# Performance work log

Measured on AMD Instinct MI355X. Metric: run time of the kernel, lower is better.

The kernel has to match this reference:

```python
import jax, jax.numpy as jnp
import numpy as np
from jax import lax

IN_CH, OUT_CH, KS, GROUPS = 64, 64, 3, 8
FPG = IN_CH // GROUPS  # features per group = 8
PAD = KS // 2


def setup_inputs() -> dict:
    key = jax.random.key(0)
    k1, k2, k3 = jax.random.split(key, 3)
    x = jax.random.normal(k1, (8, IN_CH, 256, 256), dtype=jnp.float32)
    representation = jax.random.normal(k2, (8, 32), dtype=jnp.float32)
    # Linear(32, OUT_CH*KS*KS, bias=False) weight, torch layout (out_features, in_features)
    W = jax.random.normal(k3, (OUT_CH * KS * KS, 32), dtype=jnp.float32) * (1.0 / np.sqrt(32))
    return {"x": x, "representation": representation, "W": W}


def reference(x, representation, W):
    b = x.shape[0]
    # ReflectionPad2d
    xp = jnp.pad(x, ((0, 0), (0, 0), (PAD, PAD), (PAD, PAD)), mode="reflect")
    # compress_key: Linear (no bias) + LeakyReLU(0.1)
    k = jax.nn.leaky_relu(representation @ W.T, 0.1)  # [b, OUT_CH*KS*KS]
    kernel = k.reshape(b, OUT_CH, 1, KS, KS)
    # repeat_interleave on a size-1 dim == broadcast/tile
    kernel = jnp.broadcast_to(kernel, (b, OUT_CH, FPG, KS, KS))
    # per-sample grouped conv (equivalent to torch's batch-as-groups trick)
    def conv_one(xi, ki):
        # xi: [C,H,W], ki: [OUT_CH, FPG, KS, KS]
        out = lax.conv_general_dilated(
            xi[None], ki, window_strides=(1, 1), padding="VALID",
            dimension_numbers=("NCHW", "OIHW", "NCHW"),
            feature_group_count=GROUPS)
        return out[0]
    return jax.vmap(conv_one)(xp, kernel)  # [b, OUT_CH, H, W]
```

## Files before the change

kernel.cpp:

```cpp
#include <hip/hip_runtime.h>


#define LDSW 68

__device__ __forceinline__ int reflect1(int i, int n) {
  if (i < 0) i = -i;
  if (i >= n) i = 2 * n - 2 - i;
  return i;
}

__global__ __launch_bounds__(256) void gsum_kernel(
    const float* __restrict__ x,
    float* __restrict__ S) {
  const int i = blockIdx.x * 256 + threadIdx.x;
  const int plane = i >> 14;
  const int off = i & 16383;
  const float4* p = (const float4*)x + (size_t)plane * 8 * 16384 + off;
  float4 a;
  {
    float4 v0 = p[0],         v1 = p[16384],     v2 = p[2 * 16384], v3 = p[3 * 16384];
    float4 v4 = p[4 * 16384], v5 = p[5 * 16384], v6 = p[6 * 16384], v7 = p[7 * 16384];
    a.x = ((v0.x + v1.x) + (v2.x + v3.x)) + ((v4.x + v5.x) + (v6.x + v7.x));
    a.y = ((v0.y + v1.y) + (v2.y + v3.y)) + ((v4.y + v5.y) + (v6.y + v7.y));
    a.z = ((v0.z + v1.z) + (v2.z + v3.z)) + ((v4.z + v5.z) + (v6.z + v7.z));
    a.w = ((v0.w + v1.w) + (v2.w + v3.w)) + ((v4.w + v5.w) + (v6.w + v7.w));
  }
  ((float4*)S)[i] = a;
}

#define BTH 16
__global__ __launch_bounds__(256) void dynconv3_kernel(
    const float* __restrict__ S,
    const float* __restrict__ rep,
    const float* __restrict__ W,
    float* __restrict__ out) {
  const int tid = threadIdx.x;
  const int tx = blockIdx.x & 3;
  const int ty = (blockIdx.x >> 2) & 15;
  const int g  = (blockIdx.x >> 6) & 7;
  const int b  = blockIdx.x >> 9;

  __shared__ float s[(BTH + 2) * LDSW];
  __shared__ float wl[72];

  if (tid < 72) {
    const int row = g * 72 + tid;
    const float* wr = W + (size_t)row * 32;
    const float* rb = rep + b * 32;
    float acc = 0.f;
#pragma unroll
    for (int j = 0; j < 32; ++j) acc += rb[j] * wr[j];
    wl[tid] = (acc > 0.f) ? acc : 0.1f * acc;
  }

  const int gx0 = tx * 64, gy0 = ty * BTH;
  const float* Sp = S + (size_t)(b * 8 + g) * 65536;
  const float4* Sp4 = (const float4*)Sp;

  for (int t = tid; t < 18 * 16; t += 256) {
    const int row = t >> 4, seg = t & 15;
    const int yy = reflect1(gy0 + row - 1, 256);
    float4 v = Sp4[(size_t)yy * 64 + (gx0 >> 2) + seg];
    *(float4*)&s[row * LDSW + seg * 4] = v;
  }
  if (tid < 36) {
    const int row = tid >> 1, side = tid & 1;
    const int scol = side ? 64 : 66;
    const int yy = reflect1(gy0 + row - 1, 256);
    const int xx = reflect1(gx0 + (side ? 64 : -1), 256);
    s[row * LDSW + scol] = Sp[(size_t)yy * 256 + xx];
  }
  __syncthreads();

  const int cs = (tid & 15) * 4;
  const int rr = tid >> 4;

  float win[3][6];
#pragma unroll
  for (int dy = 0; dy < 3; ++dy) {
    const float* row = &s[(rr + dy) * LDSW];
    float4 a = *(const float4*)&row[cs];
    float  r = row[cs + 4];
    float  l = row[(cs == 0) ? 66 : cs - 1];
    win[dy][0] = l;   win[dy][1] = a.x; win[dy][2] = a.y;
    win[dy][3] = a.z; win[dy][4] = a.w; win[dy][5] = r;
  }

  const int y = gy0 + rr;
  float* ob = out + (((size_t)(b * 64 + g * 8) * 256 + y) * 256 + gx0 + cs);

#pragma unroll
  for (int oc = 0; oc < 8; ++oc) {
    const float* w = &wl[oc * 9];
    const float w00 = w[0], w01 = w[1], w02 = w[2];
    const float w10 = w[3], w11 = w[4], w12 = w[5];
    const float w20 = w[6], w21 = w[7], w22 = w[8];
    float4 o;
    o.x = w00 * win[0][0] + w01 * win[0][1] + w02 * win[0][2]
        + w10 * win[1][0] + w11 * win[1][1] + w12 * win[1][2]
        + w20 * win[2][0] + w21 * win[2][1] + w22 * win[2][2];
    o.y = w00 * win[0][1] + w01 * win[0][2] + w02 * win[0][3]
        + w10 * win[1][1] + w11 * win[1][2] + w12 * win[1][3]
        + w20 * win[2][1] + w21 * win[2][2] + w22 * win[2][3];
    o.z = w00 * win[0][2] + w01 * win[0][3] + w02 * win[0][4]
        + w10 * win[1][2] + w11 * win[1][3] + w12 * win[1][4]
        + w20 * win[2][2] + w21 * win[2][3] + w22 * win[2][4];
    o.w = w00 * win[0][3] + w01 * win[0][4] + w02 * win[0][5]
        + w10 * win[1][3] + w11 * win[1][4] + w12 * win[1][5]
        + w20 * win[2][3] + w21 * win[2][4] + w22 * win[2][5];
    *(float4*)(ob + (size_t)oc * 65536) = o;
  }
}

#define TH 32
#define TW 64
__global__ __launch_bounds__(256) void dynconv_fused_kernel(
    const float* __restrict__ x, const float* __restrict__ rep,
    const float* __restrict__ W, float* __restrict__ out) {
  const int tid = threadIdx.x;
  const int tx = blockIdx.x & 3;
  const int ty = (blockIdx.x >> 2) & 7;
  const int g  = (blockIdx.x >> 5) & 7;
  const int b  = blockIdx.x >> 8;

  __shared__ float s[(TH + 2) * LDSW];
  __shared__ float wl[72];

  if (tid < 72) {
    const int row = g * 72 + tid;
    const float* wr = W + (size_t)row * 32;
    const float* rb = rep + b * 32;
    float acc = 0.f;
#pragma unroll
    for (int j = 0; j < 32; ++j) acc += rb[j] * wr[j];
    wl[tid] = (acc > 0.f) ? acc : 0.1f * acc;
  }
  __syncthreads();

  const int gx0 = tx * TW, gy0 = ty * TH;
  const float* xg = x + ((size_t)(b * 64 + g * 8)) * 65536;
  const float4* xg4 = (const float4*)xg;

  for (int t = tid; t < 34 * 16; t += 256) {
    const int row = t >> 4, seg = t & 15;
    const int yy = reflect1(gy0 + row - 1, 256);
    const float4* p = xg4 + (size_t)yy * 64 + (gx0 >> 2) + seg;
    float4 a; a.x = 0.f; a.y = 0.f; a.z = 0.f; a.w = 0.f;
#pragma unroll
    for (int c = 0; c < 8; ++c) {
      float4 v = p[(size_t)c * 16384];
      a.x += v.x; a.y += v.y; a.z += v.z; a.w += v.w;
    }
    *(float4*)&s[row * LDSW + seg * 4] = a;
  }
  if (tid < 68) {
    const int row = tid >> 1, side = tid & 1;
    const int scol = side ? 64 : 66;
    const int yy = reflect1(gy0 + row - 1, 256);
    const int xx = reflect1(gx0 + (side ? 64 : -1), 256);
    const float* p = xg + (size_t)yy * 256 + xx;
    float a = 0.f;
#pragma unroll
    for (int c = 0; c < 8; ++c) a += p[(size_t)c * 65536];
    s[row * LDSW + scol] = a;
  }
  __syncthreads();

  const int cs = (tid & 15) * 4;
  const int r0 = tid >> 4;
  for (int rr = r0; rr < TH; rr += 16) {
    float win[3][6];
#pragma unroll
    for (int dy = 0; dy < 3; ++dy) {
      const float* row = &s[(rr + dy) * LDSW];
      float4 a = *(const float4*)&row[cs];
      float  r = row[cs + 4];
      float  l = row[(cs == 0) ? 66 : cs - 1];
      win[dy][0] = l;   win[dy][1] = a.x; win[dy][2] = a.y;
      win[dy][3] = a.z; win[dy][4] = a.w; win[dy][5] = r;
    }
    const int y = gy0 + rr;
    float* ob = out + (((size_t)(b * 64 + g * 8) * 256 + y) * 256 + gx0 + cs);
#pragma unroll
    for (int oc = 0; oc < 8; ++oc) {
      const float* w = &wl[oc * 9];
      const float w00 = w[0], w01 = w[1], w02 = w[2];
      const float w10 = w[3], w11 = w[4], w12 = w[5];
      const float w20 = w[6], w21 = w[7], w22 = w[8];
      float4 o;
      o.x = w00 * win[0][0] + w01 * win[0][1] + w02 * win[0][2]
          + w10 * win[1][0] + w11 * win[1][1] + w12 * win[1][2]
          + w20 * win[2][0] + w21 * win[2][1] + w22 * win[2][2];
      o.y = w00 * win[0][1] + w01 * win[0][2] + w02 * win[0][3]
          + w10 * win[1][1] + w11 * win[1][2] + w12 * win[1][3]
          + w20 * win[2][1] + w21 * win[2][2] + w22 * win[2][3];
      o.z = w00 * win[0][2] + w01 * win[0][3] + w02 * win[0][4]
          + w10 * win[1][2] + w11 * win[1][3] + w12 * win[1][4]
          + w20 * win[2][2] + w21 * win[2][3] + w22 * win[2][4];
      o.w = w00 * win[0][3] + w01 * win[0][4] + w02 * win[0][5]
          + w10 * win[1][3] + w11 * win[1][4] + w12 * win[1][5]
          + w20 * win[2][3] + w21 * win[2][4] + w22 * win[2][5];
      *(float4*)(ob + (size_t)oc * 65536) = o;
    }
  }
}

extern "C" void kernel_launch(void* const* d_in, const int* in_sizes, int n_in,
                              void* d_out, int out_size, void* d_ws, size_t ws_size,
                              hipStream_t stream) {
  const float* x   = (const float*)d_in[0];
  const float* rep = (const float*)d_in[1];
  const float* W   = (const float*)d_in[2];
  float* out = (float*)d_out;

  const size_t s_bytes = (size_t)8 * 8 * 256 * 256 * sizeof(float);
  if (ws_size >= s_bytes) {
    float* S = (float*)d_ws;
    hipLaunchKernelGGL(gsum_kernel, dim3(4096), dim3(256), 0, stream, x, S);
    hipLaunchKernelGGL(dynconv3_kernel, dim3(4096), dim3(256), 0, stream,
                       S, rep, W, out);
  } else {
    hipLaunchKernelGGL(dynconv_fused_kernel, dim3(2048), dim3(256), 0, stream,
                       x, rep, W, out);
  }
}
```

Measured before the change: 242.6 us.

## Fuse group-sum and conv into one 512-thread kernel, drop workspace pass

Replaces the two-kernel path (group-channel sum written to workspace, then conv reading it) with one fused kernel that sums the 8 input channels straight into LDS and convolves, using 512 threads per 32x64 tile so each thread handles one output row. This removes the write and re-read of the intermediate sum buffer and one kernel launch. Weight rows are padded to stride 12 in LDS. The fused kernel has no barrier between the weight write and the tile-load barrier, but the single __syncthreads after the loads covers both.

```diff
diff --git a/kernel.cpp b/kernel.cpp
--- a/kernel.cpp
+++ b/kernel.cpp
@@ -2,6 +2,8 @@
 
 
 #define LDSW 68
+#define TH 32
+#define TW 64
 
 __device__ __forceinline__ int reflect1(int i, int n) {
   if (i < 0) i = -i;
@@ -9,66 +11,59 @@
   return i;
 }
 
-__global__ __launch_bounds__(256) void gsum_kernel(
+__global__ __launch_bounds__(512) void dynconv_fused512(
     const float* __restrict__ x,
-    float* __restrict__ S) {
-  const int i = blockIdx.x * 256 + threadIdx.x;
-  const int plane = i >> 14;
-  const int off = i & 16383;
-  const float4* p = (const float4*)x + (size_t)plane * 8 * 16384 + off;
-  float4 a;
-  {
-    float4 v0 = p[0],         v1 = p[16384],     v2 = p[2 * 16384], v3 = p[3 * 16384];
-    float4 v4 = p[4 * 16384], v5 = p[5 * 16384], v6 = p[6 * 16384], v7 = p[7 * 16384];
-    a.x = ((v0.x + v1.x) + (v2.x + v3.x)) + ((v4.x + v5.x) + (v6.x + v7.x));
-    a.y = ((v0.y + v1.y) + (v2.y + v3.y)) + ((v4.y + v5.y) + (v6.y + v7.y));
-    a.z = ((v0.z + v1.z) + (v2.z + v3.z)) + ((v4.z + v5.z) + (v6.z + v7.z));
-    a.w = ((v0.w + v1.w) + (v2.w + v3.w)) + ((v4.w + v5.w) + (v6.w + v7.w));
-  }
-  ((float4*)S)[i] = a;
-}
-
-#define BTH 16
-__global__ __launch_bounds__(256) void dynconv3_kernel(
-    const float* __restrict__ S,
     const float* __restrict__ rep,
     const float* __restrict__ W,
     float* __restrict__ out) {
   const int tid = threadIdx.x;
   const int tx = blockIdx.x & 3;
-  const int ty = (blockIdx.x >> 2) & 15;
-  const int g  = (blockIdx.x >> 6) & 7;
-  const int b  = blockIdx.x >> 9;
+  const int ty = (blockIdx.x >> 2) & 7;
+  const int g  = (blockIdx.x >> 5) & 7;
+  const int b  = blockIdx.x >> 8;
 
-  __shared__ float s[(BTH + 2) * LDSW];
-  __shared__ float wl[72];
+  __shared__ float s[(TH + 2) * LDSW];
+  __shared__ float wl[96];
 
   if (tid < 72) {
+    const int oc  = tid / 9;
+    const int tap = tid - oc * 9;
     const int row = g * 72 + tid;
     const float* wr = W + (size_t)row * 32;
     const float* rb = rep + b * 32;
     float acc = 0.f;
 #pragma unroll
     for (int j = 0; j < 32; ++j) acc += rb[j] * wr[j];
-    wl[tid] = (acc > 0.f) ? acc : 0.1f * acc;
+    wl[oc * 12 + tap] = (acc > 0.f) ? acc : 0.1f * acc;
   }
 
-  const int gx0 = tx * 64, gy0 = ty * BTH;
-  const float* Sp = S + (size_t)(b * 8 + g) * 65536;
-  const float4* Sp4 = (const float4*)Sp;
+  const int gx0 = tx * TW, gy0 = ty * TH;
+  const float* xg = x + ((size_t)(b * 64 + g * 8)) * 65536;
+  const float4* xg4 = (const float4*)xg;
 
-  for (int t = tid; t < 18 * 16; t += 256) {
+  for (int t = tid; t < 34 * 16; t += 512) {
     const int row = t >> 4, seg = t & 15;
     const int yy = reflect1(gy0 + row - 1, 256);
-    float4 v = Sp4[(size_t)yy * 64 + (gx0 >> 2) + seg];
-    *(float4*)&s[row * LDSW + seg * 4] = v;
+    const float4* p = xg4 + (size_t)yy * 64 + (gx0 >> 2) + seg;
+    float4 v0 = p[0 * 16384], v1 = p[1 * 16384], v2 = p[2 * 16384], v3 = p[3 * 16384];
+    float4 v4 = p[4 * 16384], v5 = p[5 * 16384], v6 = p[6 * 16384], v7 = p[7 * 16384];
+    float4 a;
+    a.x = ((v0.x + v1.x) + (v2.x + v3.x)) + ((v4.x + v5.x) + (v6.x + v7.x));
+    a.y = ((v0.y + v1.y) + (v2.y + v3.y)) + ((v4.y + v5.y) + (v6.y + v7.y));
+    a.z = ((v0.z + v1.z) + (v2.z + v3.z)) + ((v4.z + v5.z) + (v6.z + v7.z));
+    a.w = ((v0.w + v1.w) + (v2.w + v3.w)) + ((v4.w + v5.w) + (v6.w + v7.w));
+    *(float4*)&s[row * LDSW + seg * 4] = a;
   }
-  if (tid < 36) {
+  if (tid < 68) {
     const int row = tid >> 1, side = tid & 1;
     const int scol = side ? 64 : 66;
     const int yy = reflect1(gy0 + row - 1, 256);
     const int xx = reflect1(gx0 + (side ? 64 : -1), 256);
-    s[row * LDSW + scol] = Sp[(size_t)yy * 256 + xx];
+    const float* p = xg + (size_t)yy * 256 + xx;
+    float a = 0.f;
+#pragma unroll
+    for (int c = 0; c < 8; ++c) a += p[(size_t)c * 65536];
+    s[row * LDSW + scol] = a;
   }
   __syncthreads();
 
@@ -91,7 +86,7 @@
 
 #pragma unroll
   for (int oc = 0; oc < 8; ++oc) {
-    const float* w = &wl[oc * 9];
+    const float* w = &wl[oc * 12];
     const float w00 = w[0], w01 = w[1], w02 = w[2];
     const float w10 = w[3], w11 = w[4], w12 = w[5];
     const float w20 = w[6], w21 = w[7], w22 = w[8];
@@ -112,99 +107,6 @@
   }
 }
 
-#define TH 32
-#define TW 64
-__global__ __launch_bounds__(256) void dynconv_fused_kernel(
-    const float* __restrict__ x, const float* __restrict__ rep,
-    const float* __restrict__ W, float* __restrict__ out) {
-  const int tid = threadIdx.x;
-  const int tx = blockIdx.x & 3;
-  const int ty = (blockIdx.x >> 2) & 7;
-  const int g  = (blockIdx.x >> 5) & 7;
-  const int b  = blockIdx.x >> 8;
-
-  __shared__ float s[(TH + 2) * LDSW];
-  __shared__ float wl[72];
-
-  if (tid < 72) {
-    const int row = g * 72 + tid;
-    const float* wr = W + (size_t)row * 32;
-    const float* rb = rep + b * 32;
-    float acc = 0.f;
-#pragma unroll
-    for (int j = 0; j < 32; ++j) acc += rb[j] * wr[j];
-    wl[tid] = (acc > 0.f) ? acc : 0.1f * acc;
-  }
-  __syncthreads();
-
-  const int gx0 = tx * TW, gy0 = ty * TH;
-  const float* xg = x + ((size_t)(b * 64 + g * 8)) * 65536;
-  const float4* xg4 = (const float4*)xg;
-
-  for (int t = tid; t < 34 * 16; t += 256) {
-    const int row = t >> 4, seg = t & 15;
-    const int yy = reflect1(gy0 + row - 1, 256);
-    const float4* p = xg4 + (size_t)yy * 64 + (gx0 >> 2) + seg;
-    float4 a; a.x = 0.f; a.y = 0.f; a.z = 0.f; a.w = 0.f;
-#pragma unroll
-    for (int c = 0; c < 8; ++c) {
-      float4 v = p[(size_t)c * 16384];
-      a.x += v.x; a.y += v.y; a.z += v.z; a.w += v.w;
-    }
-    *(float4*)&s[row * LDSW + seg * 4] = a;
-  }
-  if (tid < 68) {
-    const int row = tid >> 1, side = tid & 1;
-    const int scol = side ? 64 : 66;
-    const int yy = reflect1(gy0 + row - 1, 256);
-    const int xx = reflect1(gx0 + (side ? 64 : -1), 256);
-    const float* p = xg + (size_t)yy * 256 + xx;
-    float a = 0.f;
-#pragma unroll
-    for (int c = 0; c < 8; ++c) a += p[(size_t)c * 65536];
-    s[row * LDSW + scol] = a;
-  }
-  __syncthreads();
-
-  const int cs = (tid & 15) * 4;
-  const int r0 = tid >> 4;
-  for (int rr = r0; rr < TH; rr += 16) {
-    float win[3][6];
-#pragma unroll
-    for (int dy = 0; dy < 3; ++dy) {
-      const float* row = &s[(rr + dy) * LDSW];
-      float4 a = *(const float4*)&row[cs];
-      float  r = row[cs + 4];
-      float  l = row[(cs == 0) ? 66 : cs - 1];
-      win[dy][0] = l;   win[dy][1] = a.x; win[dy][2] = a.y;
-      win[dy][3] = a.z; win[dy][4] = a.w; win[dy][5] = r;
-    }
-    const int y = gy0 + rr;
-    float* ob = out + (((size_t)(b * 64 + g * 8) * 256 + y) * 256 + gx0 + cs);
-#pragma unroll
-    for (int oc = 0; oc < 8; ++oc) {
-      const float* w = &wl[oc * 9];
-      const float w00 = w[0], w01 = w[1], w02 = w[2];
-      const float w10 = w[3], w11 = w[4], w12 = w[5];
-      const float w20 = w[6], w21 = w[7], w22 = w[8];
-      float4 o;
-      o.x = w00 * win[0][0] + w01 * win[0][1] + w02 * win[0][2]
-          + w10 * win[1][0] + w11 * win[1][1] + w12 * win[1][2]
-          + w20 * win[2][0] + w21 * win[2][1] + w22 * win[2][2];
-      o.y = w00 * win[0][1] + w01 * win[0][2] + w02 * win[0][3]
-          + w10 * win[1][1] + w11 * win[1][2] + w12 * win[1][3]
-          + w20 * win[2][1] + w21 * win[2][2] + w22 * win[2][3];
-      o.z = w00 * win[0][2] + w01 * win[0][3] + w02 * win[0][4]
-          + w10 * win[1][2] + w11 * win[1][3] + w12 * win[1][4]
-          + w20 * win[2][2] + w21 * win[2][3] + w22 * win[2][4];
-      o.w = w00 * win[0][3] + w01 * win[0][4] + w02 * win[0][5]
-          + w10 * win[1][3] + w11 * win[1][4] + w12 * win[1][5]
-          + w20 * win[2][3] + w21 * win[2][4] + w22 * win[2][5];
-      *(float4*)(ob + (size_t)oc * 65536) = o;
-    }
-  }
-}
-
 extern "C" void kernel_launch(void* const* d_in, const int* in_sizes, int n_in,
                               void* d_out, int out_size, void* d_ws, size_t ws_size,
                               hipStream_t stream) {
@@ -212,15 +114,6 @@
   const float* rep = (const float*)d_in[1];
   const float* W   = (const float*)d_in[2];
   float* out = (float*)d_out;
-
-  const size_t s_bytes = (size_t)8 * 8 * 256 * 256 * sizeof(float);
-  if (ws_size >= s_bytes) {
-    float* S = (float*)d_ws;
-    hipLaunchKernelGGL(gsum_kernel, dim3(4096), dim3(256), 0, stream, x, S);
-    hipLaunchKernelGGL(dynconv3_kernel, dim3(4096), dim3(256), 0, stream,
-                       S, rep, W, out);
-  } else {
-    hipLaunchKernelGGL(dynconv_fused_kernel, dim3(2048), dim3(256), 0, stream,
-                       x, rep, W, out);
-  }
+  hipLaunchKernelGGL(dynconv_fused512, dim3(2048), dim3(512), 0, stream,
+                     x, rep, W, out);
 }
```

Result: no change. 246.7 us (+1.7%).
